# Optimization experiments

Hardware: AMD Instinct MI355X
Metric: run time of the kernel (lower is better)

## Reference

```python
import jax, jax.numpy as jnp
import numpy as np

K = 10  # CSLS neighborhood size


def setup_inputs() -> dict:
    key = jax.random.key(0)
    k1, k2 = jax.random.split(key)
    N, D = 16384, 512
    Lvec = jax.random.normal(k1, (N, D), dtype=jnp.float32)
    Rvec = jax.random.normal(k2, (N, D), dtype=jnp.float32)
    return {"Lvec": Lvec, "Rvec": Rvec}


def reference(Lvec, Rvec):
    N = Lvec.shape[0]
    # L_sim[i, j] = <L_i, R_j>; R_sim = L_sim.T since both slices cover all rows
    sim = jnp.matmul(Lvec, Rvec.T)                      # [N_L, N_R]
    # CSLS penalties: mean of top-k similarities per row
    LR = jnp.mean(jax.lax.top_k(sim, K)[0], axis=-1)    # [N_L] per-L-entity top-k avg
    RL = jnp.mean(jax.lax.top_k(sim.T, K)[0], axis=-1)  # [N_R] per-R-entity top-k avg
    # Faithful to the torch epoch-0 broadcasting: both penalties broadcast over columns
    # csls[i, j] = 2 * R_sim[i, j] - LR[j] - RL[j]
    csls = 2.0 * sim.T - LR[None, :] - RL[None, :]      # [N_R, N_L]
    order = jnp.argsort(-csls, axis=-1)                 # descending rank lists
    # rank position of the true answer (column i for row i)
    ranks = jnp.argmax(order == jnp.arange(N)[:, None], axis=-1)  # [N] int
    top1_val = jnp.max(csls, axis=-1)                   # top-1 CSLS score per row
    return (ranks.astype(jnp.int32), top1_val)
```

## Files before the change

kernel.cpp:

```cpp
#include <hip/hip_runtime.h>
#include <hip/hip_bf16.h>
#include <hip/hip_fp8.h>
#include <stdint.h>

#define NN 16384
#define DD 512
#define BM 128
#define BN 256
#define NCT2 64
#define KT 4
#define EPW 264
#define NEG_INF (-3.0e38f)


typedef unsigned short u16;
typedef _Float16 f16;
typedef __attribute__((ext_vector_type(8))) __bf16 bf16x8;
typedef __attribute__((ext_vector_type(8))) short sh8;
typedef __attribute__((ext_vector_type(8))) _Float16 f16x8;
typedef __attribute__((ext_vector_type(4))) float f32x4;

__device__ __forceinline__ u16 f2bf(float f) {
  uint32_t x = __float_as_uint(f);
  x += 0x7fffu + ((x >> 16) & 1u);
  return (u16)(x >> 16);
}
__device__ __forceinline__ float bf2f(u16 u) {
  return __uint_as_float(((uint32_t)u) << 16);
}
__device__ __forceinline__ float f16bits(uint32_t bits) {
  f16 h;
  u16 b = (u16)bits;
  __builtin_memcpy(&h, &b, 2);
  return (float)h;
}
__device__ __forceinline__ u16 h2bits(f16 h) {
  u16 b;
  __builtin_memcpy(&b, &h, 2);
  return b;
}
__device__ __forceinline__ uint8_t f2fp8(float f) {
  __hip_fp8_e4m3 h(f);
  return (uint8_t)h.__x;
}
__device__ __forceinline__ float fp82f(uint8_t b) {
  __hip_fp8_e4m3 h;
  h.__x = (__hip_fp8_storage_t)b;
  return (float)h;
}
__device__ __forceinline__ uint32_t pk4_fp8(float a, float b, float c, float d) {
#if defined(__has_builtin) && __has_builtin(__builtin_amdgcn_cvt_pk_fp8_f32)
  int v = __builtin_amdgcn_cvt_pk_fp8_f32(a, b, 0, false);
  v = __builtin_amdgcn_cvt_pk_fp8_f32(c, d, v, true);
  return (uint32_t)v;
#else
  return (uint32_t)f2fp8(a) | ((uint32_t)f2fp8(b) << 8) |
         ((uint32_t)f2fp8(c) << 16) | ((uint32_t)f2fp8(d) << 24);
#endif
}
__device__ __forceinline__ uint32_t pk_max16(uint32_t a, uint32_t b) {
  uint32_t d;
  asm("v_pk_max_f16 %0, %1, %2" : "=v"(d) : "v"(a), "v"(b));
  return d;
}
__device__ __forceinline__ uint32_t pk_min16(uint32_t a, uint32_t b) {
  uint32_t d;
  asm("v_pk_min_f16 %0, %1, %2" : "=v"(d) : "v"(a), "v"(b));
  return d;
}

__device__ __forceinline__ void gload_lds16(const u16* g, u16* lds) {
  __builtin_amdgcn_global_load_lds(
      (const __attribute__((address_space(1))) uint32_t*)g,
      (__attribute__((address_space(3))) uint32_t*)lds,
      16, 0, 0);
}

template <int N>
__device__ __forceinline__ void insN(float (&t)[N], float v) {
  #pragma unroll
  for (int j = 0; j < N; ++j) {
    float hi = fmaxf(t[j], v);
    v = fminf(t[j], v);
    t[j] = hi;
  }
}
template <int N>
__device__ __forceinline__ void pinsN(uint32_t (&t)[N], uint32_t v) {
  #pragma unroll
  for (int j = 0; j < N; ++j) {
    uint32_t hi = pk_max16(t[j], v);
    v = pk_min16(t[j], v);
    t[j] = hi;
  }
}

__global__ __launch_bounds__(256) void cast_kernel(const float* __restrict__ src,
                                                   u16* __restrict__ dst) {
  int i = (blockIdx.x * 256 + threadIdx.x) * 8;
  const float4* s4 = reinterpret_cast<const float4*>(src + i);
  float4 a = s4[0], b = s4[1];
  sh8 o;
  o[0] = (short)f2bf(a.x); o[1] = (short)f2bf(a.y);
  o[2] = (short)f2bf(a.z); o[3] = (short)f2bf(a.w);
  o[4] = (short)f2bf(b.x); o[5] = (short)f2bf(b.y);
  o[6] = (short)f2bf(b.z); o[7] = (short)f2bf(b.w);
  *reinterpret_cast<sh8*>(dst + i) = o;
}

__global__ __launch_bounds__(256) void diag_kernel(const u16* __restrict__ Lb,
                                                   const u16* __restrict__ Rb,
                                                   float* __restrict__ diag) {
  int r = blockIdx.x * 4 + (threadIdx.x >> 6);
  int lane = threadIdx.x & 63;
  sh8 a = *reinterpret_cast<const sh8*>(Lb + (size_t)r * DD + lane * 8);
  sh8 b = *reinterpret_cast<const sh8*>(Rb + (size_t)r * DD + lane * 8);
  float s = 0.f;
  #pragma unroll
  for (int j = 0; j < 8; ++j) s += bf2f((u16)a[j]) * bf2f((u16)b[j]);
  #pragma unroll
  for (int off = 32; off > 0; off >>= 1) s += __shfl_down(s, off);
  if (lane == 0) diag[r] = s;
}

#define DECODE_TILE(ct0)                                \
  const int xcd = blockIdx.x & 7;                       \
  const int idx = blockIdx.x >> 3;                      \
  const int rowtile = xcd * 16 + (idx & 15);            \
  const int coltile = (ct0) + (idx >> 4);               \
  const int rowbase = rowtile * BM;                     \
  const int colbase = coltile * BN;                     \
  const int tid = threadIdx.x;                          \
  const int w = tid >> 6;                               \
  const int lane = tid & 63;                            \
  const int quad = lane >> 4;                           \
  const int l16 = lane & 15;                            \
  const int wr = (w >> 2) * 64;                         \
  const int wc = (w & 3) * 64;                          \
  (void)xcd; (void)lane;

#define GEMM_PRE()                                                              \
  const int rp0_ = tid >> 3, gp0_ = (tid & 7) ^ (rp0_ & 7);                     \
  const int grow0_ = rp0_ * 2 + (gp0_ >> 2), gcol0_ = (gp0_ & 3) * 8;           \
  const int gl1_ = tid + 512;                                                   \
  const int rp1_ = gl1_ >> 3, gp1_ = (gl1_ & 7) ^ (rp1_ & 7);                   \
  const int grow1_ = rp1_ * 2 + (gp1_ >> 2), gcol1_ = (gp1_ & 3) * 8;           \
  const u16* gA_  = A + (size_t)(rowbase + grow0_) * DD + gcol0_;               \
  const u16* gB0_ = B + (size_t)(colbase + grow0_) * DD + gcol0_;               \
  const u16* gB1_ = B + (size_t)(colbase + grow1_) * DD + gcol1_;               \
  const int gsel_ = ((((l16) & 1) << 2) + quad) ^ (l16 >> 1);                   \
  const int rdA_ = (wr / 2 + (l16 >> 1)) * 64 + gsel_ * 8;                      \
  const int rdB_ = (wc / 2 + (l16 >> 1)) * 64 + gsel_ * 8;

#define STAGE(t, dA, dB)                                                        \
  gload_lds16(gA_  + (t) * 32, (dA) + tid * 8);                                 \
  gload_lds16(gB0_ + (t) * 32, (dB) + tid * 8);                                 \
  gload_lds16(gB1_ + (t) * 32, (dB) + 4096 + tid * 8);

#define GEMM_K_LOOP(sA0_, sA1_, sB0_, sB1_)                                     \
  f32x4 acc[4][4];                                                              \
  _Pragma("unroll")                                                             \
  for (int a_ = 0; a_ < 4; ++a_)                                                \
    _Pragma("unroll")                                                           \
    for (int b_ = 0; b_ < 4; ++b_) acc[a_][b_] = (f32x4){0.f, 0.f, 0.f, 0.f};   \
  {                                                                             \
    GEMM_PRE()                                                                  \
    u16* const bufA_[2] = {(sA0_), (sA1_)};                                     \
    u16* const bufB_[2] = {(sB0_), (sB1_)};                                     \
    STAGE(0, bufA_[0], bufB_[0])                                                \
    STAGE(1, bufA_[1], bufB_[1])                                                \
    _Pragma("unroll")                                                           \
    for (int t = 0; t < 16; ++t) {                                              \
      if (t < 15) { asm volatile("s_waitcnt vmcnt(3)" ::: "memory"); }          \
      else        { asm volatile("s_waitcnt vmcnt(0)" ::: "memory"); }          \
      __builtin_amdgcn_s_barrier();                                             \
      asm volatile("" ::: "memory");                                            \
      {                                                                         \
        const u16* cA_ = bufA_[t & 1];                                          \
        const u16* cB_ = bufB_[t & 1];                                          \
        bf16x8 af[4], bfv[4];                                                   \
        _Pragma("unroll")                                                       \
        for (int f = 0; f < 4; ++f)                                             \
          af[f]  = *reinterpret_cast<const bf16x8*>(cA_ + rdA_ + f * 512);      \
        _Pragma("unroll")                                                       \
        for (int f = 0; f < 4; ++f)                                             \
          bfv[f] = *reinterpret_cast<const bf16x8*>(cB_ + rdB_ + f * 512);      \
        _Pragma("unroll")                                                       \
        for (int fr = 0; fr < 4; ++fr)                                          \
          _Pragma("unroll")                                                     \
          for (int fc = 0; fc < 4; ++fc)                                        \
            acc[fr][fc] = __builtin_amdgcn_mfma_f32_16x16x32_bf16(af[fr], bfv[fc], acc[fr][fc], 0, 0, 0); \
      }                                                                         \
      asm volatile("" ::: "memory");                                            \
      __builtin_amdgcn_s_barrier();                                             \
      if (t + 2 < 16) { STAGE(t + 2, bufA_[t & 1], bufB_[t & 1]) }              \
    }                                                                           \
  }

__global__ __launch_bounds__(512, 4) void gemm_topk(const u16* __restrict__ A,
                                                    const u16* __restrict__ B,
                                                    f16* __restrict__ rowp,
                                                    f16* __restrict__ colp,
                                                    uint8_t* __restrict__ sim,
                                                    int SC2) {
  __shared__ __align__(16) u16 smem[33792];
  u16* sA0 = smem;
  u16* sA1 = smem + 4096;
  u16* sB0 = smem + 8192;
  u16* sB1 = smem + 16384;
  DECODE_TILE(0)
  GEMM_K_LOOP(sA0, sA1, sB0, sB1)

  f16* hC = reinterpret_cast<f16*>(smem);
  #pragma unroll
  for (int fr = 0; fr < 4; ++fr)
    #pragma unroll
    for (int fc = 0; fc < 4; ++fc)
      #pragma unroll
      for (int reg = 0; reg < 4; ++reg)
        hC[(wr + 16 * fr + quad * 4 + reg) * EPW + wc + 16 * fc + l16] =
            (f16)acc[fr][fc][reg];
  __syncthreads();
  if (coltile < SC2) {
    const int SW = SC2 * BN;
    uint8_t* gs = sim + (size_t)rowbase * SW + (size_t)coltile * BN;
    #pragma unroll
    for (int itw = 0; itw < 8; ++itw) {
      int idx2 = itw * 4096 + tid * 8;
      int rr = idx2 >> 8, cc = idx2 & 255;
      f16x8 v = *reinterpret_cast<const f16x8*>(hC + rr * EPW + cc);
      uint2 o;
      o.x = pk4_fp8((float)v[0], (float)v[1], (float)v[2], (float)v[3]);
      o.y = pk4_fp8((float)v[4], (float)v[5], (float)v[6], (float)v[7]);
      *reinterpret_cast<uint2*>(gs + (size_t)rr * SW + cc) = o;
    }
  }
  uint32_t trow[KT];
  #pragma unroll
  for (int j = 0; j < KT; ++j) trow[j] = 0xFBFFFBFFu;
  {
    const u16* q = reinterpret_cast<const u16*>(hC) + (tid >> 2) * EPW + (tid & 3) * 64;
    #pragma unroll
    for (int c8 = 0; c8 < 8; ++c8) {
      uint4 ch = *reinterpret_cast<const uint4*>(q + c8 * 8);
      pinsN<KT>(trow, ch.x);
      pinsN<KT>(trow, ch.y);
      pinsN<KT>(trow, ch.z);
      pinsN<KT>(trow, ch.w);
    }
  }
  uint32_t tcol[KT];
  #pragma unroll
  for (int j = 0; j < KT; ++j) tcol[j] = 0xFBFFFBFFu;
  const int cp = tid & 127, rq = tid >> 7;
  {
    const u16* base = reinterpret_cast<const u16*>(hC) + rq * 32 * EPW + 2 * cp;
    #pragma unroll 8
    for (int i = 0; i < 32; ++i) {
      uint32_t v = *reinterpret_cast<const uint32_t*>(base + i * EPW);
      pinsN<KT>(tcol, v);
    }
  }
  __syncthreads();
  uint32_t* sCl = reinterpret_cast<uint32_t*>(smem);
  uint32_t* sRl = reinterpret_cast<uint32_t*>(smem) + 128 * 4 * KT;
  #pragma unroll
  for (int j = 0; j < KT; ++j) sCl[(cp * 4 + rq) * KT + j] = tcol[j];
  #pragma unroll
  for (int j = 0; j < KT; ++j) sRl[tid * KT + j] = trow[j];
  __syncthreads();
  if (tid < 256) {
    float best[KT];
    #pragma unroll
    for (int j = 0; j < KT; ++j) best[j] = NEG_INF;
    const int cpp = tid >> 1, par = tid & 1;
    for (int rqi = 0; rqi < 4; ++rqi)
      for (int j = 0; j < KT; ++j) {
        uint32_t u = sCl[(cpp * 4 + rqi) * KT + j];
        float v = f16bits(par ? (u >> 16) : u);
        if (v > best[KT - 1]) insN<KT>(best, v);
        else break;
      }
    f16* o = colp + ((size_t)rowtile * NN + colbase + tid) * KT;
    uint2 ov;
    ov.x = h2bits((f16)best[0]) | ((uint32_t)h2bits((f16)best[1]) << 16);
    ov.y = h2bits((f16)best[2]) | ((uint32_t)h2bits((f16)best[3]) << 16);
    *reinterpret_cast<uint2*>(o) = ov;
  } else if (tid < 384) {
    const int r = tid - 256;
    float best[KT];
    #pragma unroll
    for (int j = 0; j < KT; ++j) best[j] = NEG_INF;
    for (int h = 0; h < 4; ++h)
      for (int par = 0; par < 2; ++par)
        for (int j = 0; j < KT; ++j) {
          uint32_t u = sRl[(r * 4 + h) * KT + j];
          float v = f16bits(par ? (u >> 16) : u);
          if (v > best[KT - 1]) insN<KT>(best, v);
          else break;
        }
    f16* o = rowp + ((size_t)coltile * NN + rowbase + r) * KT;
    uint2 ov;
    ov.x = h2bits((f16)best[0]) | ((uint32_t)h2bits((f16)best[1]) << 16);
    ov.y = h2bits((f16)best[2]) | ((uint32_t)h2bits((f16)best[3]) << 16);
    *reinterpret_cast<uint2*>(o) = ov;
  }
}

__global__ __launch_bounds__(512, 4) void gemm_rank(const u16* __restrict__ A,
                                                    const u16* __restrict__ B,
                                                    const float* __restrict__ p,
                                                    const float* __restrict__ thr,
                                                    int* __restrict__ cnt_out,
                                                    float* __restrict__ mx_out,
                                                    int ct0) {
  __shared__ __align__(16) u16 smem[24576];
  u16* sA0 = smem;
  u16* sA1 = smem + 4096;
  u16* sB0 = smem + 8192;
  u16* sB1 = smem + 16384;
  DECODE_TILE(ct0)

  GEMM_K_LOOP(sA0, sA1, sB0, sB1)

  float thrv[16];
  #pragma unroll
  for (int i = 0; i < 16; ++i)
    thrv[i] = thr[rowbase + wr + 16 * (i >> 2) + quad * 4 + (i & 3)];
  float pv[4];
  #pragma unroll
  for (int fc = 0; fc < 4; ++fc) pv[fc] = p[colbase + wc + 16 * fc + l16];

  int cnt[16];
  float mx[16];
  #pragma unroll
  for (int i = 0; i < 16; ++i) { cnt[i] = 0; mx[i] = NEG_INF; }
  #pragma unroll
  for (int fc = 0; fc < 4; ++fc)
    #pragma unroll
    for (int fr = 0; fr < 4; ++fr)
      #pragma unroll
      for (int reg = 0; reg < 4; ++reg) {
        float t2 = 2.f * acc[fr][fc][reg] - pv[fc];
        int idx2 = fr * 4 + reg;
        cnt[idx2] += (t2 > thrv[idx2]) ? 1 : 0;
        mx[idx2] = fmaxf(mx[idx2], t2);
      }

  float* sMx = reinterpret_cast<float*>(smem);
  int*   sCn = reinterpret_cast<int*>(smem) + 512;
  #pragma unroll
  for (int idx2 = 0; idx2 < 16; ++idx2) {
    int c = cnt[idx2];
    float m = mx[idx2];
    #pragma unroll
    for (int off = 1; off < 16; off <<= 1) {
      c += __shfl_xor(c, off);
      m = fmaxf(m, __shfl_xor(m, off));
    }
    if (l16 == 0) {
      int rloc = 16 * (idx2 >> 2) + quad * 4 + (idx2 & 3);
      sMx[w * 64 + rloc] = m;
      sCn[w * 64 + rloc] = c;
    }
  }
  __syncthreads();
  if (tid < 128) {
    int g0 = (tid >> 6) * 4, rloc = tid & 63;
    int c = 0;
    float m = NEG_INF;
    #pragma unroll
    for (int k = 0; k < 4; ++k) {
      c += sCn[(g0 + k) * 64 + rloc];
      m = fmaxf(m, sMx[(g0 + k) * 64 + rloc]);
    }
    cnt_out[(size_t)coltile * NN + rowbase + tid] = c;
    mx_out[(size_t)coltile * NN + rowbase + tid] = m;
  }
}

__global__ __launch_bounds__(256) void scan_kernel(const uint8_t* __restrict__ sim,
                                                   const float* __restrict__ p,
                                                   const float* __restrict__ thr,
                                                   int SC2,
                                                   int* __restrict__ cnt_s,
                                                   float* __restrict__ mx_s) {
  const int tid = threadIdx.x;
  const int row0 = blockIdx.x * 4;
  const int SW = SC2 * BN;
  float t[4];
  #pragma unroll
  for (int r = 0; r < 4; ++r) t[r] = thr[row0 + r];
  int cnt[4] = {0, 0, 0, 0};
  float m[4] = {NEG_INF, NEG_INF, NEG_INF, NEG_INF};
  for (int c0 = tid * 16; c0 < SW; c0 += 4096) {
    float pv[16];
    {
      const float4* p4 = reinterpret_cast<const float4*>(p + c0);
      *reinterpret_cast<float4*>(&pv[0])  = p4[0];
      *reinterpret_cast<float4*>(&pv[4])  = p4[1];
      *reinterpret_cast<float4*>(&pv[8])  = p4[2];
      *reinterpret_cast<float4*>(&pv[12]) = p4[3];
    }
    #pragma unroll
    for (int r = 0; r < 4; ++r) {
      uint4 v = *reinterpret_cast<const uint4*>(sim + (size_t)(row0 + r) * SW + c0);
      uint32_t wds[4] = {v.x, v.y, v.z, v.w};
      #pragma unroll
      for (int j = 0; j < 16; ++j) {
        float sv = fp82f((uint8_t)(wds[j >> 2] >> ((j & 3) * 8)));
        float t2 = 2.f * sv - pv[j];
        cnt[r] += (t2 > t[r]) ? 1 : 0;
        m[r] = fmaxf(m[r], t2);
      }
    }
  }
  __shared__ float sM[4][4];
  __shared__ int sC[4][4];
  const int lane = tid & 63, w = tid >> 6;
  #pragma unroll
  for (int r = 0; r < 4; ++r) {
    int c = cnt[r];
    float mm = m[r];
    #pragma unroll
    for (int off = 32; off > 0; off >>= 1) {
      c += __shfl_down(c, off);
      mm = fmaxf(mm, __shfl_down(mm, off));
    }
    if (lane == 0) { sC[r][w] = c; sM[r][w] = mm; }
  }
  __syncthreads();
  if (tid < 4) {
    int c = sC[tid][0] + sC[tid][1] + sC[tid][2] + sC[tid][3];
    float mm = fmaxf(fmaxf(sM[tid][0], sM[tid][1]), fmaxf(sM[tid][2], sM[tid][3]));
    cnt_s[row0 + tid] = c;
    mx_s[row0 + tid] = mm;
  }
}

__global__ __launch_bounds__(256) void p_kernel(const f16* __restrict__ rowp,
                                                const f16* __restrict__ colp,
                                                const float* __restrict__ diag,
                                                float* __restrict__ pout,
                                                float* __restrict__ throut) {
  __shared__ float sB1[64][4][10];
  __shared__ float sB2[64][4][10];
  const int tid = threadIdx.x;
  const int lent = tid >> 2, part = tid & 3;
  const int l = blockIdx.x * 64 + lent;
  float b1[10], b2[10];
  #pragma unroll
  for (int j = 0; j < 10; ++j) { b1[j] = NEG_INF; b2[j] = NEG_INF; }
  for (int s = part * 16; s < part * 16 + 16; ++s) {
    uint2 u2 = *reinterpret_cast<const uint2*>(rowp + ((size_t)s * NN + l) * KT);
    uint32_t ud[2] = {u2.x, u2.y};
    #pragma unroll
    for (int d = 0; d < 2; ++d) {
      uint32_t u = ud[d];
      float v0 = f16bits(u), v1 = f16bits(u >> 16);
      if (v0 > b1[9]) insN<10>(b1, v0); else break;
      if (v1 > b1[9]) insN<10>(b1, v1); else break;
    }
  }
  for (int s = part * 32; s < part * 32 + 32; ++s) {
    uint2 u2 = *reinterpret_cast<const uint2*>(colp + ((size_t)s * NN + l) * KT);
    uint32_t ud[2] = {u2.x, u2.y};
    #pragma unroll
    for (int d = 0; d < 2; ++d) {
      uint32_t u = ud[d];
      float v0 = f16bits(u), v1 = f16bits(u >> 16);
      if (v0 > b2[9]) insN<10>(b2, v0); else break;
      if (v1 > b2[9]) insN<10>(b2, v1); else break;
    }
  }
  #pragma unroll
  for (int j = 0; j < 10; ++j) { sB1[lent][part][j] = b1[j]; sB2[lent][part][j] = b2[j]; }
  __syncthreads();
  if (tid < 64) {
    const int l2 = blockIdx.x * 64 + tid;
    float m1[10], m2[10];
    #pragma unroll
    for (int j = 0; j < 10; ++j) { m1[j] = NEG_INF; m2[j] = NEG_INF; }
    for (int pa = 0; pa < 4; ++pa) {
      for (int j = 0; j < 10; ++j) {
        float v = sB1[tid][pa][j];
        if (v > m1[9]) insN<10>(m1, v); else break;
      }
      for (int j = 0; j < 10; ++j) {
        float v = sB2[tid][pa][j];
        if (v > m2[9]) insN<10>(m2, v); else break;
      }
    }
    float s1 = 0.f, s2 = 0.f;
    #pragma unroll
    for (int j = 0; j < 10; ++j) { s1 += m1[j]; s2 += m2[j]; }
    float pv = (s1 + s2) * 0.1f;
    pout[l2] = pv;
    throut[l2] = 2.f * diag[l2] - pv;
  }
}

__global__ __launch_bounds__(256) void final_kernel(const int* __restrict__ cnt,
                                                    const float* __restrict__ mx,
                                                    const int* __restrict__ cnt_s,
                                                    const float* __restrict__ mx_s,
                                                    int sc2,
                                                    float* __restrict__ out) {
  int r = blockIdx.x * 256 + threadIdx.x;
  int c = 0;
  float m = NEG_INF;
  if (sc2 > 0) { c = cnt_s[r]; m = mx_s[r]; }
  for (int s = sc2; s < NCT2; ++s) {
    c += cnt[(size_t)s * NN + r];
    m = fmaxf(m, mx[(size_t)s * NN + r]);
  }
  out[r] = (float)c;
  out[NN + r] = m;
}

extern "C" void kernel_launch(void* const* d_in, const int* in_sizes, int n_in,
                              void* d_out, int out_size, void* d_ws, size_t ws_size,
                              hipStream_t stream) {
  const float* L = (const float*)d_in[0];
  const float* R = (const float*)d_in[1];
  char* ws = (char*)d_ws;

  const size_t PART_ROW = (size_t)NCT2 * NN * KT * 2;
  const size_t PART_COL = (size_t)128 * NN * KT * 2;
  const size_t TAILOFF = (32ull << 20) + PART_ROW + PART_COL;
  const size_t SIMOFF = TAILOFF + (320ull << 10);

  u16* Lb   = (u16*)ws;
  u16* Rb   = (u16*)(ws + (16ull << 20));
  f16* rowp = (f16*)(ws + (32ull << 20));
  f16* colp = (f16*)(ws + (32ull << 20) + PART_ROW);
  char* tail = ws + TAILOFF;
  float* diag   = (float*)tail;
  float* pbuf   = (float*)(tail + (64ull << 10));
  float* thrbuf = (float*)(tail + (128ull << 10));
  int*   cnt_s  = (int*)(tail + (192ull << 10));
  float* mx_s   = (float*)(tail + (256ull << 10));
  uint8_t* sim  = (uint8_t*)(ws + SIMOFF);
  int*   cntp = (int*)rowp;
  float* mxp  = (float*)colp;

  int SC2 = 0;
  if (ws_size > SIMOFF) {
    size_t sc = (ws_size - SIMOFF) / ((size_t)NN * BN * 1);
    if (sc > 64) sc = 64;
    SC2 = (int)sc;
  }

  cast_kernel<<<(NN * DD / (256 * 8)), 256, 0, stream>>>(L, Lb);
  cast_kernel<<<(NN * DD / (256 * 8)), 256, 0, stream>>>(R, Rb);
  diag_kernel<<<NN / 4, 256, 0, stream>>>(Lb, Rb, diag);
  gemm_topk<<<(NN / BM) * NCT2, 512, 0, stream>>>(Rb, Lb, rowp, colp, sim, SC2);
  p_kernel<<<NN / 64, 256, 0, stream>>>(rowp, colp, diag, pbuf, thrbuf);
  if (SC2 > 0)
    scan_kernel<<<NN / 4, 256, 0, stream>>>(sim, pbuf, thrbuf, SC2, cnt_s, mx_s);
  if (SC2 < NCT2)
    gemm_rank<<<(NN / BM) * (NCT2 - SC2), 512, 0, stream>>>(Rb, Lb, pbuf, thrbuf,
                                                            cntp, mxp, SC2);
  final_kernel<<<NN / 256, 256, 0, stream>>>(cntp, mxp, cnt_s, mx_s, SC2,
                                             (float*)d_out);
}
```

Measured before the change: 580.6 us.

## Triple-buffer GEMM K-loop, drop second barrier, pack f16 epilogue by row pairs

The GEMM K-loop moves from two LDS stages to three rotating buffers, so the barrier after each MFMA block can go. The next prefetch now writes a buffer that no wave is still reading. MFMA issue is wrapped in s_setprio to favor the compute waves. The epilogue packs pairs of rows into 32-bit f16 words with v_cvt_pkrtz and reorganizes the fp8 store and the row and column top-k scans around this layout, which should reduce LDS traffic and conversions. The cost is more LDS per block (72KB), which may lower occupancy at launch_bounds(512,4), and f16 rounding changes from nearest to round-toward-zero.

```diff
diff --git a/kernel.cpp b/kernel.cpp
--- a/kernel.cpp
+++ b/kernel.cpp
@@ -9,7 +9,7 @@
 #define BN 256
 #define NCT2 64
 #define KT 4
-#define EPW 264
+#define PPW 260
 #define NEG_INF (-3.0e38f)
 
 
@@ -57,6 +57,11 @@
   return (uint32_t)f2fp8(a) | ((uint32_t)f2fp8(b) << 8) |
          ((uint32_t)f2fp8(c) << 16) | ((uint32_t)f2fp8(d) << 24);
 #endif
+}
+__device__ __forceinline__ uint32_t pkrtz(float a, float b) {
+  uint32_t d;
+  asm("v_cvt_pkrtz_f16_f32 %0, %1, %2" : "=v"(d) : "v"(a), "v"(b));
+  return d;
 }
 __device__ __forceinline__ uint32_t pk_max16(uint32_t a, uint32_t b) {
   uint32_t d;
@@ -157,7 +162,7 @@
   gload_lds16(gB0_ + (t) * 32, (dB) + tid * 8);                                 \
   gload_lds16(gB1_ + (t) * 32, (dB) + 4096 + tid * 8);
 
-#define GEMM_K_LOOP(sA0_, sA1_, sB0_, sB1_)                                     \
+#define GEMM_K_LOOP(smembase)                                                   \
   f32x4 acc[4][4];                                                              \
   _Pragma("unroll")                                                             \
   for (int a_ = 0; a_ < 4; ++a_)                                                \
@@ -165,10 +170,11 @@
     for (int b_ = 0; b_ < 4; ++b_) acc[a_][b_] = (f32x4){0.f, 0.f, 0.f, 0.f};   \
   {                                                                             \
     GEMM_PRE()                                                                  \
-    u16* const bufA_[2] = {(sA0_), (sA1_)};                                     \
-    u16* const bufB_[2] = {(sB0_), (sB1_)};                                     \
-    STAGE(0, bufA_[0], bufB_[0])                                                \
-    STAGE(1, bufA_[1], bufB_[1])                                                \
+    u16* const bA_[3] = {(smembase), (smembase) + 4096, (smembase) + 8192};     \
+    u16* const bB_[3] = {(smembase) + 12288, (smembase) + 20480,                \
+                         (smembase) + 28672};                                   \
+    STAGE(0, bA_[0], bB_[0])                                                    \
+    STAGE(1, bA_[1], bB_[1])                                                    \
     _Pragma("unroll")                                                           \
     for (int t = 0; t < 16; ++t) {                                              \
       if (t < 15) { asm volatile("s_waitcnt vmcnt(3)" ::: "memory"); }          \
@@ -176,8 +182,9 @@
       __builtin_amdgcn_s_barrier();                                             \
       asm volatile("" ::: "memory");                                            \
       {                                                                         \
-        const u16* cA_ = bufA_[t & 1];                                          \
-        const u16* cB_ = bufB_[t & 1];                                          \
+        const int cs_ = t % 3;                                                  \
+        const u16* cA_ = bA_[cs_];                                              \
+        const u16* cB_ = bB_[cs_];                                              \
         bf16x8 af[4], bfv[4];                                                   \
         _Pragma("unroll")                                                       \
         for (int f = 0; f < 4; ++f)                                             \
@@ -185,15 +192,19 @@
         _Pragma("unroll")                                                       \
         for (int f = 0; f < 4; ++f)                                             \
           bfv[f] = *reinterpret_cast<const bf16x8*>(cB_ + rdB_ + f * 512);      \
+        __builtin_amdgcn_s_setprio(1);                                          \
         _Pragma("unroll")                                                       \
         for (int fr = 0; fr < 4; ++fr)                                          \
           _Pragma("unroll")                                                     \
           for (int fc = 0; fc < 4; ++fc)                                        \
             acc[fr][fc] = __builtin_amdgcn_mfma_f32_16x16x32_bf16(af[fr], bfv[fc], acc[fr][fc], 0, 0, 0); \
+        __builtin_amdgcn_s_setprio(0);                                          \
       }                                                                         \
       asm volatile("" ::: "memory");                                            \
-      __builtin_amdgcn_s_barrier();                                             \
-      if (t + 2 < 16) { STAGE(t + 2, bufA_[t & 1], bufB_[t & 1]) }              \
+      if (t + 2 < 16) {                                                         \
+        const int ns_ = (t + 2) % 3;                                            \
+        STAGE(t + 2, bA_[ns_], bB_[ns_])                                        \
+      }                                                                         \
     }                                                                           \
   }
 
@@ -203,84 +214,80 @@
                                                     f16* __restrict__ colp,
                                                     uint8_t* __restrict__ sim,
                                                     int SC2) {
-  __shared__ __align__(16) u16 smem[33792];
-  u16* sA0 = smem;
-  u16* sA1 = smem + 4096;
-  u16* sB0 = smem + 8192;
-  u16* sB1 = smem + 16384;
+  __shared__ __align__(16) u16 smem[36864];
   DECODE_TILE(0)
-  GEMM_K_LOOP(sA0, sA1, sB0, sB1)
-
-  f16* hC = reinterpret_cast<f16*>(smem);
-  #pragma unroll
-  for (int fr = 0; fr < 4; ++fr)
-    #pragma unroll
-    for (int fc = 0; fc < 4; ++fc)
-      #pragma unroll
-      for (int reg = 0; reg < 4; ++reg)
-        hC[(wr + 16 * fr + quad * 4 + reg) * EPW + wc + 16 * fc + l16] =
-            (f16)acc[fr][fc][reg];
+  GEMM_K_LOOP(smem)
+
+  __syncthreads();
+  uint32_t* hC32 = reinterpret_cast<uint32_t*>(smem);
+  #pragma unroll
+  for (int fr = 0; fr < 4; ++fr) {
+    const int rpb = (wr + 16 * fr) / 2 + quad * 2;
+    #pragma unroll
+    for (int fc = 0; fc < 4; ++fc) {
+      const int c = wc + 16 * fc + l16;
+      hC32[rpb * PPW + c]       = pkrtz(acc[fr][fc][0], acc[fr][fc][1]);
+      hC32[(rpb + 1) * PPW + c] = pkrtz(acc[fr][fc][2], acc[fr][fc][3]);
+    }
+  }
   __syncthreads();
   if (coltile < SC2) {
     const int SW = SC2 * BN;
     uint8_t* gs = sim + (size_t)rowbase * SW + (size_t)coltile * BN;
+    const int rp0s = tid >> 6, cb = tid & 63;
     #pragma unroll
     for (int itw = 0; itw < 8; ++itw) {
-      int idx2 = itw * 4096 + tid * 8;
-      int rr = idx2 >> 8, cc = idx2 & 255;
-      f16x8 v = *reinterpret_cast<const f16x8*>(hC + rr * EPW + cc);
-      uint2 o;
-      o.x = pk4_fp8((float)v[0], (float)v[1], (float)v[2], (float)v[3]);
-      o.y = pk4_fp8((float)v[4], (float)v[5], (float)v[6], (float)v[7]);
-      *reinterpret_cast<uint2*>(gs + (size_t)rr * SW + cc) = o;
+      const int rp = rp0s + itw * 8;
+      uint4 v = *reinterpret_cast<const uint4*>(&hC32[rp * PPW + cb * 4]);
+      uint32_t d0 = v.x, d1 = v.y, d2 = v.z, d3 = v.w;
+      uint32_t r0 = pk4_fp8(f16bits(d0), f16bits(d1), f16bits(d2), f16bits(d3));
+      uint32_t r1 = pk4_fp8(f16bits(d0 >> 16), f16bits(d1 >> 16),
+                            f16bits(d2 >> 16), f16bits(d3 >> 16));
+      *reinterpret_cast<uint32_t*>(gs + (size_t)(2 * rp) * SW + cb * 4) = r0;
+      *reinterpret_cast<uint32_t*>(gs + (size_t)(2 * rp + 1) * SW + cb * 4) = r1;
     }
   }
   uint32_t trow[KT];
   #pragma unroll
   for (int j = 0; j < KT; ++j) trow[j] = 0xFBFFFBFFu;
-  {
-    const u16* q = reinterpret_cast<const u16*>(hC) + (tid >> 2) * EPW + (tid & 3) * 64;
-    #pragma unroll
-    for (int c8 = 0; c8 < 8; ++c8) {
-      uint4 ch = *reinterpret_cast<const uint4*>(q + c8 * 8);
-      pinsN<KT>(trow, ch.x);
-      pinsN<KT>(trow, ch.y);
-      pinsN<KT>(trow, ch.z);
-      pinsN<KT>(trow, ch.w);
-    }
+  const int rsp = tid >> 3, ce = tid & 7;
+  #pragma unroll
+  for (int k = 0; k < 8; ++k) {
+    uint4 ch = *reinterpret_cast<const uint4*>(&hC32[rsp * PPW + ce * 32 + k * 4]);
+    pinsN<KT>(trow, ch.x);
+    pinsN<KT>(trow, ch.y);
+    pinsN<KT>(trow, ch.z);
+    pinsN<KT>(trow, ch.w);
   }
   uint32_t tcol[KT];
   #pragma unroll
   for (int j = 0; j < KT; ++j) tcol[j] = 0xFBFFFBFFu;
-  const int cp = tid & 127, rq = tid >> 7;
-  {
-    const u16* base = reinterpret_cast<const u16*>(hC) + rq * 32 * EPW + 2 * cp;
-    #pragma unroll 8
-    for (int i = 0; i < 32; ++i) {
-      uint32_t v = *reinterpret_cast<const uint32_t*>(base + i * EPW);
-      pinsN<KT>(tcol, v);
-    }
-  }
-  __syncthreads();
-  uint32_t* sCl = reinterpret_cast<uint32_t*>(smem);
-  uint32_t* sRl = reinterpret_cast<uint32_t*>(smem) + 128 * 4 * KT;
-  #pragma unroll
-  for (int j = 0; j < KT; ++j) sCl[(cp * 4 + rq) * KT + j] = tcol[j];
-  #pragma unroll
-  for (int j = 0; j < KT; ++j) sRl[tid * KT + j] = trow[j];
+  const int cc = tid & 255, rph = tid >> 8;
+  #pragma unroll 8
+  for (int i = 0; i < 32; ++i) {
+    uint32_t v = hC32[(rph * 32 + i) * PPW + cc];
+    pinsN<KT>(tcol, v);
+  }
+  __syncthreads();
+  uint32_t* sRl = hC32;
+  uint32_t* sCl = hC32 + 64 * 8 * KT;
+  #pragma unroll
+  for (int j = 0; j < KT; ++j) sRl[(rsp * 8 + ce) * KT + j] = trow[j];
+  #pragma unroll
+  for (int j = 0; j < KT; ++j) sCl[(cc * 2 + rph) * KT + j] = tcol[j];
   __syncthreads();
   if (tid < 256) {
     float best[KT];
     #pragma unroll
     for (int j = 0; j < KT; ++j) best[j] = NEG_INF;
-    const int cpp = tid >> 1, par = tid & 1;
-    for (int rqi = 0; rqi < 4; ++rqi)
-      for (int j = 0; j < KT; ++j) {
-        uint32_t u = sCl[(cpp * 4 + rqi) * KT + j];
-        float v = f16bits(par ? (u >> 16) : u);
-        if (v > best[KT - 1]) insN<KT>(best, v);
-        else break;
-      }
+    for (int rh = 0; rh < 2; ++rh)
+      for (int par = 0; par < 2; ++par)
+        for (int j = 0; j < KT; ++j) {
+          uint32_t u = sCl[(tid * 2 + rh) * KT + j];
+          float v = f16bits(par ? (u >> 16) : u);
+          if (v > best[KT - 1]) insN<KT>(best, v);
+          else break;
+        }
     f16* o = colp + ((size_t)rowtile * NN + colbase + tid) * KT;
     uint2 ov;
     ov.x = h2bits((f16)best[0]) | ((uint32_t)h2bits((f16)best[1]) << 16);
@@ -288,17 +295,17 @@
     *reinterpret_cast<uint2*>(o) = ov;
   } else if (tid < 384) {
     const int r = tid - 256;
+    const int rp = r >> 1, par = r & 1;
     float best[KT];
     #pragma unroll
     for (int j = 0; j < KT; ++j) best[j] = NEG_INF;
-    for (int h = 0; h < 4; ++h)
-      for (int par = 0; par < 2; ++par)
-        for (int j = 0; j < KT; ++j) {
-          uint32_t u = sRl[(r * 4 + h) * KT + j];
-          float v = f16bits(par ? (u >> 16) : u);
-          if (v > best[KT - 1]) insN<KT>(best, v);
-          else break;
-        }
+    for (int h = 0; h < 8; ++h)
+      for (int j = 0; j < KT; ++j) {
+        uint32_t u = sRl[(rp * 8 + h) * KT + j];
+        float v = f16bits(par ? (u >> 16) : u);
+        if (v > best[KT - 1]) insN<KT>(best, v);
+        else break;
+      }
     f16* o = rowp + ((size_t)coltile * NN + rowbase + r) * KT;
     uint2 ov;
     ov.x = h2bits((f16)best[0]) | ((uint32_t)h2bits((f16)best[1]) << 16);
@@ -314,14 +321,10 @@
                                                     int* __restrict__ cnt_out,
                                                     float* __restrict__ mx_out,
                                                     int ct0) {
-  __shared__ __align__(16) u16 smem[24576];
-  u16* sA0 = smem;
-  u16* sA1 = smem + 4096;
-  u16* sB0 = smem + 8192;
-  u16* sB1 = smem + 16384;
+  __shared__ __align__(16) u16 smem[36864];
   DECODE_TILE(ct0)
 
-  GEMM_K_LOOP(sA0, sA1, sB0, sB1)
+  GEMM_K_LOOP(smem)
 
   float thrv[16];
   #pragma unroll
@@ -347,6 +350,7 @@
         mx[idx2] = fmaxf(mx[idx2], t2);
       }
 
+  __syncthreads();
   float* sMx = reinterpret_cast<float*>(smem);
   int*   sCn = reinterpret_cast<int*>(smem) + 512;
   #pragma unroll
```

Result: no change. 569.3 us (-1.9%).
